# Optimization experiments

Measured on AMD Instinct MI355X. Metric: run time of the kernel, lower is better.

## Reference

```python
import jax, jax.numpy as jnp
import numpy as np

H = 128  # hidden_size

def _band_agg(h):
    # Equivalent to bmm(adj, h) with adj = degree-normalized tridiagonal
    # (self + left + right neighbor), degree=3 interior, 2 at endpoints,
    # normalization adj/(deg+1e-8) as in the torch module.
    B, S, D = h.shape
    hp = jnp.pad(h, ((0, 0), (1, 1), (0, 0)))
    s = hp[:, :-2] + hp[:, 1:-1] + hp[:, 2:]            # [B,S,D] neighbor sum
    deg = jnp.full((S,), 3.0, dtype=h.dtype).at[0].set(2.0).at[S - 1].set(2.0)
    return s / (deg + 1e-8)[None, :, None]


def setup_inputs() -> dict:
    key = jax.random.key(0)
    ks = jax.random.split(key, 16)
    f32 = jnp.float32
    p = lambda k, shp: (jax.random.normal(k, shp, dtype=f32) * 0.05)
    return {
        "x": jax.random.normal(ks[0], (32, 2048, 6), dtype=f32),
        "enc_w1": p(ks[1], (6, H)),   "enc_b1": p(ks[2], (H,)),
        "enc_w2": p(ks[3], (H, H)),   "enc_b2": p(ks[4], (H,)),
        "gc1_w": p(ks[5], (H, H)),    "gc1_b": p(ks[6], (H,)),
        "gc2_w": p(ks[7], (H, H)),    "gc2_b": p(ks[8], (H,)),
        "gc3_w": p(ks[9], (H, H)),    "gc3_b": p(ks[10], (H,)),
        "cls_w1": p(ks[11], (H, H // 2)), "cls_b1": p(ks[12], (H // 2,)),
        "cls_w2": p(ks[13], (H // 2, 3)), "cls_b2": p(ks[14], (3,)),
    }


def reference(x, enc_w1, enc_b1, enc_w2, enc_b2,
              gc1_w, gc1_b, gc2_w, gc2_b, gc3_w, gc3_b,
              cls_w1, cls_b1, cls_w2, cls_b2):
    # node encoder: Linear -> ReLU -> Linear
    h = jax.nn.relu(x @ enc_w1 + enc_b1) @ enc_w2 + enc_b2
    # three graph convolutions: linear, normalized tridiagonal aggregate, relu
    h = jax.nn.relu(_band_agg(h @ gc1_w + gc1_b))
    h = jax.nn.relu(_band_agg(h @ gc2_w + gc2_b))
    h = jax.nn.relu(_band_agg(h @ gc3_w + gc3_b))
    # AdaptiveAvgPool1d(1) over seq dim after transpose == mean over nodes
    pooled = h.mean(axis=1)                              # [B, H]
    # classifier (dropout inactive in eval)
    return jax.nn.relu(pooled @ cls_w1 + cls_b1) @ cls_w2 + cls_b2
```

## Files before the change

### kernel.cpp

```cpp
#include <hip/hip_runtime.h>

#define SEQ  2048
#define HID  128
#define NB   32
#define TILE 58
#define GX   36
#define MSTR 67

typedef float f2     __attribute__((ext_vector_type(2)));
typedef float f32x4  __attribute__((ext_vector_type(4)));
typedef short bf16x8 __attribute__((ext_vector_type(8)));

__device__ __forceinline__ void split_bf16(float v, short& h, short& l) {
  unsigned u = __float_as_uint(v);
  unsigned r = (u + 0x7fffu + ((u >> 16) & 1u)) >> 16;
  h = (short)r;
  const float hf = __uint_as_float(r << 16);
  const float lo = v - hf;
  unsigned u2 = __float_as_uint(lo);
  unsigned r2 = (u2 + 0x7fffu + ((u2 >> 16) & 1u)) >> 16;
  l = (short)r2;
}

__device__ __forceinline__ short cvt_bf16(float v) {
  unsigned u = __float_as_uint(v);
  return (short)((u + 0x7fffu + ((u >> 16) & 1u)) >> 16);
}

__global__ __launch_bounds__(256) void prep_kernel(
    const float* __restrict__ enc_w2, const float* __restrict__ enc_b2,
    const float* __restrict__ gc1_w, const float* __restrict__ gc1_b,
    const float* __restrict__ gc2_w, const float* __restrict__ gc3_w,
    short* __restrict__ Wf, float* __restrict__ bp)
{
  __shared__ float Wls[32][130];
  __shared__ float ew2s[32][128];
  __shared__ float bsum[2][128];

  const int ks = blockIdx.x;
  const int L  = blockIdx.y;
  const int tid = threadIdx.x;

  if (L == 0) {
    for (int f = tid; f < 32 * 128; f += 256)
      ew2s[f >> 7][f & 127] = enc_w2[(ks * 32 + (f >> 7)) * 128 + (f & 127)];
    __syncthreads();
    {
      const int c = tid & 127, rh = tid >> 7;
      float acc[16];
      #pragma unroll
      for (int i = 0; i < 16; ++i) acc[i] = 0.f;
      #pragma unroll 4
      for (int k = 0; k < 128; ++k) {
        const float g = gc1_w[k * 128 + c];
        #pragma unroll
        for (int i = 0; i < 16; ++i)
          acc[i] = fmaf(ew2s[rh * 16 + i][k], g, acc[i]);
      }
      #pragma unroll
      for (int i = 0; i < 16; ++i) Wls[rh * 16 + i][c] = acc[i];
    }
    if (ks == 0) {
      const int c = tid & 127, kh = tid >> 7;
      float s = 0.f;
      #pragma unroll 4
      for (int k0 = 0; k0 < 64; ++k0) {
        const int k = kh * 64 + k0;
        s = fmaf(enc_b2[k], gc1_w[k * 128 + c], s);
      }
      bsum[kh][c] = s;
    }
    __syncthreads();
    if (ks == 0 && tid < 128) bp[tid] = gc1_b[tid] + bsum[0][tid] + bsum[1][tid];
  } else {
    const float* SW = (L == 1) ? gc2_w : gc3_w;
    for (int f = tid; f < 32 * 128; f += 256)
      Wls[f >> 7][f & 127] = SW[(ks * 32 + (f >> 7)) * 128 + (f & 127)];
    __syncthreads();
  }

  short* hi = Wf + L * 32768 + ks * 4096;
  short* lo = hi + 16384;
  for (int f = tid; f < 4096; f += 256) {
    const int nt = f >> 9, l = (f >> 3) & 63, j = f & 7;
    const int kk = (l >> 4) * 8 + j;
    const int n  = nt * 16 + (l & 15);
    short h, lw;
    split_bf16(Wls[kk][n], h, lw);
    hi[f] = h; lo[f] = lw;
  }
}

__global__ __launch_bounds__(256) void fused_kernel(
    const float* __restrict__ x,
    const float* __restrict__ enc_w1, const float* __restrict__ enc_b1,
    const short* __restrict__ Wf, const float* __restrict__ bp,
    const float* __restrict__ gc2_b, const float* __restrict__ gc3_b,
    float* __restrict__ partial)
{
  __shared__ float hT[HID * MSTR];
  __shared__ float wsmall[7 * HID];
  __shared__ float psum[256];

  const int tid  = threadIdx.x;
  const int lane = tid & 63;
  const int w    = tid >> 6;
  const int gxb  = blockIdx.x, b = blockIdx.y;
  const int s0   = gxb * TILE;

  for (int f = tid; f < 7 * HID; f += 256)
    wsmall[f] = (f < 6 * HID) ? enc_w1[f] : enc_b1[f - 6 * HID];

  const int sm = s0 - 3 + lane;
  float xv[6];
  if (sm >= 0 && sm < SEQ) {
    const f2* xp = (const f2*)(x + ((long long)b * SEQ + sm) * 6);
    const f2 a0 = xp[0], a1 = xp[1], a2 = xp[2];
    xv[0] = a0.x; xv[1] = a0.y; xv[2] = a1.x;
    xv[3] = a1.y; xv[4] = a2.x; xv[5] = a2.y;
  } else {
    #pragma unroll
    for (int k = 0; k < 6; ++k) xv[k] = 0.f;
  }
  __syncthreads();
  {
    const int c0 = w * 32;
    float4 a4[8];
    #pragma unroll
    for (int q = 0; q < 8; ++q) a4[q] = make_float4(0.f, 0.f, 0.f, 0.f);
    #pragma unroll
    for (int k = 0; k < 6; ++k) {
      #pragma unroll
      for (int q = 0; q < 8; ++q) {
        const float4 wv = *(const float4*)&wsmall[k * HID + c0 + q * 4];
        a4[q].x = fmaf(xv[k], wv.x, a4[q].x);
        a4[q].y = fmaf(xv[k], wv.y, a4[q].y);
        a4[q].z = fmaf(xv[k], wv.z, a4[q].z);
        a4[q].w = fmaf(xv[k], wv.w, a4[q].w);
      }
    }
    #pragma unroll
    for (int q = 0; q < 8; ++q) {
      const float4 bb = *(const float4*)&wsmall[6 * HID + c0 + q * 4];
      const int c = c0 + q * 4;
      hT[(c + 0) * MSTR + lane] = fmaxf(a4[q].x + bb.x, 0.f);
      hT[(c + 1) * MSTR + lane] = fmaxf(a4[q].y + bb.y, 0.f);
      hT[(c + 2) * MSTR + lane] = fmaxf(a4[q].z + bb.z, 0.f);
      hT[(c + 3) * MSTR + lane] = fmaxf(a4[q].w + bb.w, 0.f);
    }
  }
  __syncthreads();

  const int mt   = w * 16 + (lane & 15);
  const int koct = (lane >> 4) * 8;
  const int stt  = s0 - 3 + mt;
  const float invdA = (stt == 0 || stt == SEQ - 1) ? (1.0f / (2.0f + 1e-8f))
                                                   : (1.0f / (3.0f + 1e-8f));
  const int mm = (mt == 0) ? 0 : mt - 1;
  const int mp = (mt == 63) ? 63 : mt + 1;

  #pragma unroll 1
  for (int L = 0; L < 3; ++L) {
    const short* WfL = Wf + L * 32768;
    const bf16x8* Bhi = (const bf16x8*)WfL;
    const bf16x8* Blo = (const bf16x8*)(WfL + 16384);
    const float* bias = (L == 0) ? bp : (L == 1) ? gc2_b : gc3_b;

    f32x4 acc[8];
    #pragma unroll
    for (int nt = 0; nt < 8; ++nt) acc[nt] = (f32x4){0.f, 0.f, 0.f, 0.f};

    #pragma unroll 1
    for (int ks = 0; ks < 4; ++ks) {
      const int fb = ks * 512 + lane;
      bf16x8 bh[8], bl[8];
      #pragma unroll
      for (int nt = 0; nt < 8; ++nt) {
        bh[nt] = Bhi[fb + nt * 64];
        bl[nt] = Blo[fb + nt * 64];
      }
      bf16x8 ah;
      const float* pa = &hT[(ks * 32 + koct) * MSTR];
      #pragma unroll
      for (int j = 0; j < 8; ++j) {
        float v;
        if (L == 0) {
          v = pa[j * MSTR + mt];
        } else {
          v = (pa[j * MSTR + mm] + pa[j * MSTR + mt] + pa[j * MSTR + mp]) * invdA;
          v = fmaxf(v, 0.f);
        }
        ah[j] = cvt_bf16(v);
      }
      #pragma unroll
      for (int nt = 0; nt < 8; ++nt) {
        acc[nt] = __builtin_amdgcn_mfma_f32_16x16x32_bf16(ah, bh[nt], acc[nt], 0, 0, 0);
        acc[nt] = __builtin_amdgcn_mfma_f32_16x16x32_bf16(ah, bl[nt], acc[nt], 0, 0, 0);
      }
    }
    __syncthreads();

    {
      const int n0 = lane & 15;
      const int mrow0 = w * 16 + (lane >> 4) * 4;
      #pragma unroll
      for (int nt = 0; nt < 8; ++nt) {
        const float bn = bias[nt * 16 + n0];
        float* pw = &hT[(nt * 16 + n0) * MSTR];
        #pragma unroll
        for (int r = 0; r < 4; ++r) {
          const int m = mrow0 + r;
          const int s = s0 - 3 + m;
          const bool vld = (s >= 0 && s < SEQ);
          pw[m] = vld ? (acc[nt][r] + bn) : 0.f;
        }
      }
    }
    __syncthreads();
  }

  {
    const int c = tid & 127, half = tid >> 7;
    float ps = 0.f;
    const float* pc = &hT[c * MSTR];
    #pragma unroll 1
    for (int r = 0; r < 29; ++r) {
      const int m = 3 + half * 29 + r;
      const int s = s0 + half * 29 + r;
      if (s < SEQ) {
        const float invd = (s == 0 || s == SEQ - 1) ? (1.0f / (2.0f + 1e-8f))
                                                    : (1.0f / (3.0f + 1e-8f));
        ps += fmaxf((pc[m - 1] + pc[m] + pc[m + 1]) * invd, 0.f);
      }
    }
    psum[tid] = ps;
  }
  __syncthreads();
  if (tid < 128)
    partial[((long long)b * GX + gxb) * HID + tid] = psum[tid] + psum[tid + 128];
}

__global__ __launch_bounds__(256) void cls_kernel(
    const float* __restrict__ partial,
    const float* __restrict__ w1, const float* __restrict__ b1,
    const float* __restrict__ w2, const float* __restrict__ b2,
    float* __restrict__ out)
{
  __shared__ float red[256];
  __shared__ float ms[128];
  __shared__ float hp[4][64];
  __shared__ float hid[64];
  const int b = blockIdx.x, tid = threadIdx.x;

  {
    const int c = tid & 127, gh = tid >> 7;
    float a = 0.f;
    #pragma unroll 2
    for (int g = gh; g < GX; g += 2)
      a += partial[((long long)b * GX + g) * HID + c];
    red[tid] = a;
  }
  __syncthreads();
  if (tid < 128) ms[tid] = (red[tid] + red[tid + 128]) * (1.0f / 2048.0f);
  __syncthreads();
  {
    const int c = tid & 63, kq = tid >> 6;
    float h = 0.f;
    #pragma unroll 8
    for (int k0 = 0; k0 < 32; ++k0) {
      const int k = kq * 32 + k0;
      h = fmaf(ms[k], w1[k * 64 + c], h);
    }
    hp[kq][c] = h;
  }
  __syncthreads();
  if (tid < 64)
    hid[tid] = fmaxf(hp[0][tid] + hp[1][tid] + hp[2][tid] + hp[3][tid] + b1[tid], 0.f);
  __syncthreads();
  if (tid < 3) {
    float o = b2[tid];
    #pragma unroll 8
    for (int k = 0; k < 64; ++k) o = fmaf(hid[k], w2[k * 3 + tid], o);
    out[b * 3 + tid] = o;
  }
}

extern "C" void kernel_launch(void* const* d_in, const int* in_sizes, int n_in,
                              void* d_out, int out_size, void* d_ws, size_t ws_size,
                              hipStream_t stream) {
  (void)in_sizes; (void)n_in; (void)out_size; (void)ws_size;
  const float* x      = (const float*)d_in[0];
  const float* enc_w1 = (const float*)d_in[1];
  const float* enc_b1 = (const float*)d_in[2];
  const float* enc_w2 = (const float*)d_in[3];
  const float* enc_b2 = (const float*)d_in[4];
  const float* gc1_w  = (const float*)d_in[5];
  const float* gc1_b  = (const float*)d_in[6];
  const float* gc2_w  = (const float*)d_in[7];
  const float* gc2_b  = (const float*)d_in[8];
  const float* gc3_w  = (const float*)d_in[9];
  const float* gc3_b  = (const float*)d_in[10];
  const float* cls_w1 = (const float*)d_in[11];
  const float* cls_b1 = (const float*)d_in[12];
  const float* cls_w2 = (const float*)d_in[13];
  const float* cls_b2 = (const float*)d_in[14];

  short* Wfrag   = (short*)d_ws;
  float* bpv     = (float*)(Wfrag + 3 * 2 * 16384);
  float* partial = bpv + 128;

  prep_kernel<<<dim3(4, 3), 256, 0, stream>>>(
      enc_w2, enc_b2, gc1_w, gc1_b, gc2_w, gc3_w, Wfrag, bpv);
  fused_kernel<<<dim3(GX, NB), 256, 0, stream>>>(
      x, enc_w1, enc_b1, Wfrag, bpv, gc2_b, gc3_b, partial);
  cls_kernel<<<dim3(NB), 256, 0, stream>>>(partial, cls_w1, cls_b1, cls_w2, cls_b2,
                                           (float*)d_out);
}
```

Measured before the change: 150.4 us.

## Fuse classifier into main kernel via last-blocks atomic counter

```diff
diff --git a/kernel.cpp b/kernel.cpp
--- a/kernel.cpp
+++ b/kernel.cpp
@@ -5,6 +5,7 @@
 #define NB   32
 #define TILE 58
 #define GX   36
+#define NTILES (GX * NB)
 #define MSTR 67
 
 typedef float f2     __attribute__((ext_vector_type(2)));
@@ -27,11 +28,16 @@
   return (short)((u + 0x7fffu + ((u >> 16) & 1u)) >> 16);
 }
 
+__device__ __forceinline__ float cohload(const float* p) {
+  return __hip_atomic_load(p, __ATOMIC_RELAXED, __HIP_MEMORY_SCOPE_AGENT);
+}
+
 __global__ __launch_bounds__(256) void prep_kernel(
     const float* __restrict__ enc_w2, const float* __restrict__ enc_b2,
     const float* __restrict__ gc1_w, const float* __restrict__ gc1_b,
     const float* __restrict__ gc2_w, const float* __restrict__ gc3_w,
-    short* __restrict__ Wf, float* __restrict__ bp)
+    short* __restrict__ Wf, float* __restrict__ bp,
+    unsigned* __restrict__ counter)
 {
   __shared__ float Wls[32][130];
   __shared__ float ew2s[32][128];
@@ -41,6 +47,9 @@
   const int L  = blockIdx.y;
   const int tid = threadIdx.x;
 
+  if (L == 2 && ks == 0 && tid == 0)
+    __hip_atomic_store(counter, 0u, __ATOMIC_RELEASE, __HIP_MEMORY_SCOPE_AGENT);
+
   if (L == 0) {
     for (int f = tid; f < 32 * 128; f += 256)
       ew2s[f >> 7][f & 127] = enc_w2[(ks * 32 + (f >> 7)) * 128 + (f & 127)];
@@ -50,7 +59,7 @@
       float acc[16];
       #pragma unroll
       for (int i = 0; i < 16; ++i) acc[i] = 0.f;
-      #pragma unroll 4
+      #pragma unroll 8
       for (int k = 0; k < 128; ++k) {
         const float g = gc1_w[k * 128 + c];
         #pragma unroll
@@ -63,7 +72,7 @@
     if (ks == 0) {
       const int c = tid & 127, kh = tid >> 7;
       float s = 0.f;
-      #pragma unroll 4
+      #pragma unroll 8
       for (int k0 = 0; k0 < 64; ++k0) {
         const int k = kh * 64 + k0;
         s = fmaf(enc_b2[k], gc1_w[k * 128 + c], s);
@@ -96,11 +105,15 @@
     const float* __restrict__ enc_w1, const float* __restrict__ enc_b1,
     const short* __restrict__ Wf, const float* __restrict__ bp,
     const float* __restrict__ gc2_b, const float* __restrict__ gc3_b,
-    float* __restrict__ partial)
+    float* __restrict__ partial, unsigned* __restrict__ counter,
+    const float* __restrict__ cls_w1, const float* __restrict__ cls_b1,
+    const float* __restrict__ cls_w2, const float* __restrict__ cls_b2,
+    float* __restrict__ out)
 {
   __shared__ float hT[HID * MSTR];
   __shared__ float wsmall[7 * HID];
   __shared__ float psum[256];
+  __shared__ int mybs;
 
   const int tid  = threadIdx.x;
   const int lane = tid & 63;
@@ -238,50 +251,61 @@
   __syncthreads();
   if (tid < 128)
     partial[((long long)b * GX + gxb) * HID + tid] = psum[tid] + psum[tid + 128];
-}
-
-__global__ __launch_bounds__(256) void cls_kernel(
-    const float* __restrict__ partial,
-    const float* __restrict__ w1, const float* __restrict__ b1,
-    const float* __restrict__ w2, const float* __restrict__ b2,
-    float* __restrict__ out)
-{
-  __shared__ float red[256];
-  __shared__ float ms[128];
-  __shared__ float hp[4][64];
-  __shared__ float hid[64];
-  const int b = blockIdx.x, tid = threadIdx.x;
+  __syncthreads();
+
+  if (tid == 0) {
+    __threadfence();
+    const unsigned old = __hip_atomic_fetch_add(counter, 1u, __ATOMIC_ACQ_REL,
+                                                __HIP_MEMORY_SCOPE_AGENT);
+    mybs = (old >= NTILES - 32) ? (int)(old - (NTILES - 32)) : -1;
+  }
+  __syncthreads();
+  const int cb = mybs;
+  if (cb < 0) return;
+
+  if (tid == 0) {
+    while (__hip_atomic_load(counter, __ATOMIC_ACQUIRE,
+                             __HIP_MEMORY_SCOPE_AGENT) < (unsigned)NTILES) {}
+  }
+  __syncthreads();
 
   {
-    const int c = tid & 127, gh = tid >> 7;
-    float a = 0.f;
-    #pragma unroll 2
-    for (int g = gh; g < GX; g += 2)
-      a += partial[((long long)b * GX + g) * HID + c];
-    red[tid] = a;
-  }
-  __syncthreads();
-  if (tid < 128) ms[tid] = (red[tid] + red[tid + 128]) * (1.0f / 2048.0f);
-  __syncthreads();
-  {
-    const int c = tid & 63, kq = tid >> 6;
-    float h = 0.f;
-    #pragma unroll 8
-    for (int k0 = 0; k0 < 32; ++k0) {
-      const int k = kq * 32 + k0;
-      h = fmaf(ms[k], w1[k * 64 + c], h);
-    }
-    hp[kq][c] = h;
-  }
-  __syncthreads();
-  if (tid < 64)
-    hid[tid] = fmaxf(hp[0][tid] + hp[1][tid] + hp[2][tid] + hp[3][tid] + b1[tid], 0.f);
-  __syncthreads();
-  if (tid < 3) {
-    float o = b2[tid];
-    #pragma unroll 8
-    for (int k = 0; k < 64; ++k) o = fmaf(hid[k], w2[k * 3 + tid], o);
-    out[b * 3 + tid] = o;
+    float* red = hT;
+    float* ms  = hT + 256;
+    float* hp  = hT + 384;
+    float* hid = hT + 640;
+    {
+      const int c = tid & 127, gh = tid >> 7;
+      float a = 0.f;
+      #pragma unroll 2
+      for (int g = gh; g < GX; g += 2)
+        a += cohload(&partial[((long long)cb * GX + g) * HID + c]);
+      red[tid] = a;
+    }
+    __syncthreads();
+    if (tid < 128) ms[tid] = (red[tid] + red[tid + 128]) * (1.0f / 2048.0f);
+    __syncthreads();
+    {
+      const int c = tid & 63, kq = tid >> 6;
+      float h = 0.f;
+      #pragma unroll 8
+      for (int k0 = 0; k0 < 32; ++k0) {
+        const int k = kq * 32 + k0;
+        h = fmaf(ms[k], cls_w1[k * 64 + c], h);
+      }
+      hp[kq * 64 + c] = h;
+    }
+    __syncthreads();
+    if (tid < 64)
+      hid[tid] = fmaxf(hp[tid] + hp[64 + tid] + hp[128 + tid] + hp[192 + tid]
+                       + cls_b1[tid], 0.f);
+    __syncthreads();
+    if (tid < 3) {
+      float o = cls_b2[tid];
+      #pragma unroll 8
+      for (int k = 0; k < 64; ++k) o = fmaf(hid[k], cls_w2[k * 3 + tid], o);
+      out[cb * 3 + tid] = o;
+    }
   }
 }
 
@@ -305,14 +329,14 @@
   const float* cls_w2 = (const float*)d_in[13];
   const float* cls_b2 = (const float*)d_in[14];
 
-  short* Wfrag   = (short*)d_ws;
-  float* bpv     = (float*)(Wfrag + 3 * 2 * 16384);
-  float* partial = bpv + 128;
+  short* Wfrag     = (short*)d_ws;
+  float* bpv       = (float*)(Wfrag + 3 * 2 * 16384);
+  float* partial   = bpv + 128;
+  unsigned* counter = (unsigned*)(partial + (size_t)NB * GX * HID);
 
   prep_kernel<<<dim3(4, 3), 256, 0, stream>>>(
-      enc_w2, enc_b2, gc1_w, gc1_b, gc2_w, gc3_w, Wfrag, bpv);
+      enc_w2, enc_b2, gc1_w, gc1_b, gc2_w, gc3_w, Wfrag, bpv, counter);
   fused_kernel<<<dim3(GX, NB), 256, 0, stream>>>(
-      x, enc_w1, enc_b1, Wfrag, bpv, gc2_b, gc3_b, partial);
-  cls_kernel<<<dim3(NB), 256, 0, stream>>>(partial, cls_w1, cls_b1, cls_w2, cls_b2,
-                                           (float*)d_out);
-}
+      x, enc_w1, enc_b1, Wfrag, bpv, gc2_b, gc3_b, partial, counter,
+      cls_w1, cls_b1, cls_w2, cls_b2, (float*)d_out);
+}
```

New measurement: 207.2 us. 37.8% more time.
